# Optimization experiments

Hardware: AMD Instinct MI355X
Metric: run time of the kernel (lower is better)

The kernel has to match this reference:

```python
import jax, jax.numpy as jnp
import numpy as np

B, T, V, E, H, NL = 32, 64, 32000, 300, 512, 2
NF, D = 128, 32  # num midi frames, midi_frame_dim
LSTM_IN = E + D  # 332


def setup_inputs() -> dict:
    key = jax.random.key(0)
    ks = jax.random.split(key, 20)
    s = 0.05
    inp = {
        "input_seq": jax.random.randint(ks[0], (B, T), 0, V),
        "midi_sequence": jax.random.normal(ks[1], (B, NF, D), jnp.float32),
        "emb": jax.random.normal(ks[2], (V, E), jnp.float32) * s,
        "mp_w": jax.random.normal(ks[3], (D, D), jnp.float32) * s,
        "mp_b": jnp.zeros((D,), jnp.float32),
        "wh": jax.random.normal(ks[4], (H, H), jnp.float32) * s,
        "wm": jax.random.normal(ks[5], (H, D), jnp.float32) * s,
        "v": jax.random.normal(ks[6], (1, H), jnp.float32) * s,
        "w_ih0": jax.random.normal(ks[7], (4 * H, LSTM_IN), jnp.float32) * s,
        "w_hh0": jax.random.normal(ks[8], (4 * H, H), jnp.float32) * s,
        "b_ih0": jnp.zeros((4 * H,), jnp.float32),
        "b_hh0": jnp.zeros((4 * H,), jnp.float32),
        "w_ih1": jax.random.normal(ks[9], (4 * H, H), jnp.float32) * s,
        "w_hh1": jax.random.normal(ks[10], (4 * H, H), jnp.float32) * s,
        "b_ih1": jnp.zeros((4 * H,), jnp.float32),
        "b_hh1": jnp.zeros((4 * H,), jnp.float32),
        "fc_w": jax.random.uniform(ks[11], (V, H), jnp.float32, -0.1, 0.1),
        "fc_b": jnp.zeros((V,), jnp.float32),
    }
    return inp


def _lstm_cell(x, hp, cp, wih, whh, bih, bhh):
    # PyTorch gate order: i, f, g, o
    g = x @ wih.T + hp @ whh.T + bih + bhh
    i, f, gg, o = jnp.split(g, 4, axis=-1)
    cn = jax.nn.sigmoid(f) * cp + jax.nn.sigmoid(i) * jnp.tanh(gg)
    hn = jax.nn.sigmoid(o) * jnp.tanh(cn)
    return hn, cn


def reference(input_seq, midi_sequence, emb, mp_w, mp_b, wh, wm, v,
              w_ih0, w_hh0, b_ih0, b_hh0, w_ih1, w_hh1, b_ih1, b_hh1,
              fc_w, fc_b):
    embeddings = emb[input_seq]  # [B,T,E] (dropout = identity in eval)
    midi_proj = jax.nn.relu(jnp.einsum('bfd,ed->bfe', midi_sequence, mp_w) + mp_b)  # [B,NF,D]
    midi_key = jnp.einsum('bfd,hd->bfh', midi_proj, wm)  # precomputed W_m(midi_proj)

    h0 = jnp.zeros((NL, B, H), embeddings.dtype)
    c0 = jnp.zeros((NL, B, H), embeddings.dtype)

    def step(carry, x_t):
        h, c = carry
        h_top = h[-1]  # [B,H]
        energy = jnp.tanh((h_top @ wh.T)[:, None, :] + midi_key)  # [B,NF,H]
        scores = jnp.einsum('bfh,h->bf', energy, v[0])
        attn = jax.nn.softmax(scores, axis=-1)  # [B,NF]
        ctx = jnp.einsum('bf,bfd->bd', attn, midi_proj)  # [B,D]
        x = jnp.concatenate([x_t, ctx], axis=-1)  # [B,E+D]
        h1, c1 = _lstm_cell(x, h[0], c[0], w_ih0, w_hh0, b_ih0, b_hh0)
        h2, c2 = _lstm_cell(h1, h[1], c[1], w_ih1, w_hh1, b_ih1, b_hh1)
        return (jnp.stack([h1, h2]), jnp.stack([c1, c2])), (h2, attn)

    (hF, cF), (outs, attns) = jax.lax.scan(step, (h0, c0), embeddings.transpose(1, 0, 2))
    lstm_out = outs.transpose(1, 0, 2)  # [B,T,H]
    logits = lstm_out @ fc_w.T + fc_b  # [B,T,V]
    return logits, (hF, cF), attns.transpose(1, 0, 2)
```

## Files before the change

### kernel.cpp

```cpp
#include <hip/hip_runtime.h>
#include <hip/hip_bf16.h>

#define Bsz 32
#define Tn  64
#define Vn  32000
#define En  300
#define Hn  512
#define NFn 128
#define Dn  32
#define G4  2048
#define LIN 332
#define NWG 256

#define OFF_MPROJ 0
#define OFF_E0    (OFF_MPROJ + 131072)
#define OFF_PG0B  (OFF_E0 + 4194304)
#define OFF_H1T   (OFF_PG0B + 65536)
#define OFF_H2T0  (OFF_H1T + 16384)
#define OFF_H2T1  (OFF_H2T0 + 16384)
#define OFF_H2BB  (OFF_H2T1 + 16384)
#define OFF_C1T   (OFF_H2BB + 16384)
#define OFF_C2T   (OFF_C1T + 16384)
#define OFF_FLG   (OFF_C2T + 16384)
#define OFF_DONE  (OFF_FLG + 4096)
#define OFF_VC    (OFF_DONE + 256)
#define OFF_MKEY  (OFF_VC + 16)
#define OFF_WHT   (OFF_MKEY + 2097152)
#define OFF_WCTX  (OFF_WHT + 262144)
#define OFF_X     (OFF_WCTX + 65536)
#define OFF_W0    (OFF_X + 655360)
#define OFF_HBF   OFF_X
#define OFF_FCWBF (OFF_X + 524288)

#define O_H1S 0
#define O_H2S 1048576

#define OFF_QS    OFF_PG0B
#define OFF_CTXP  (OFF_PG0B + 16384)
#define OFF_DENP  (OFF_PG0B + 24576)
#define OFF_ES    (OFF_PG0B + 24832)

#define OUT_HF  65536000
#define OUT_CF  65568768
#define OUT_ATT 65601536

#define L_HS2   0
#define L_HS1   4096
#define L_GL    8192
#define L_PG0   8480
#define L_C1    8736
#define L_C2    8800
#define L_CTX   8864
#define L_DEN   9128
#define L_QL    9136
#define L_VL    9664
#define L_SP    10192
#define L_ESL   10464
#define L_CP    10480
#define SCAN_LDS_FLOATS 11024
#define SCAN_LDS_BYTES  (SCAN_LDS_FLOATS*4)

typedef __attribute__((ext_vector_type(8))) short short8;
typedef __attribute__((ext_vector_type(4))) float f32x4;
typedef unsigned short u16;

__device__ __forceinline__ float frcp(float x){ return __builtin_amdgcn_rcpf(x); }
__device__ __forceinline__ float ftanh(float x){
  float e = __expf(2.0f*x);
  return 1.0f - 2.0f*frcp(e+1.0f);
}
__device__ __forceinline__ float fsig(float x){
  return frcp(1.0f + __expf(-x));
}
__device__ __forceinline__ u16 f2bf(float f){
  __hip_bfloat16 h = __float2bfloat16(f);
  u16 r; __builtin_memcpy(&r, &h, 2); return r;
}

__device__ __forceinline__ float ldc1(const float* p){
  return __hip_atomic_load(p, __ATOMIC_RELAXED, __HIP_MEMORY_SCOPE_AGENT);
}
__device__ __forceinline__ void stc1(float* p, float v){
  __hip_atomic_store(p, v, __ATOMIC_RELAXED, __HIP_MEMORY_SCOPE_AGENT);
}

__device__ __forceinline__ void flag_store(float* ws, int c, int slot, float v){
  stc1(ws + OFF_FLG + c*256 + slot*4, v);
}
__device__ __forceinline__ void aggregate(float* ws, int c, float tgt, int tid){
  if (tid < 64){
    const float* fl = ws + OFF_FLG + c*256;
    unsigned cc = 0;
    while (true){
      float v = ldc1(fl + tid*4);
      if (__ballot(v >= tgt) == ~0ull) break;
      __builtin_amdgcn_s_sleep(2);
      if (++cc >= (1u<<20)) break;
    }
    if (tid == 0) stc1(ws + OFF_DONE + c*16, tgt);
  }
}
__device__ __forceinline__ void waitD(float* ws, int c, float tgt){
  __syncthreads();
  if (threadIdx.x == 0){
    unsigned cc = 0;
    while (ldc1(ws + OFF_DONE + c*16) < tgt){
      __builtin_amdgcn_s_sleep(2);
      if (++cc >= (1u<<22)) break;
    }
  }
  __syncthreads();
  asm volatile("" ::: "memory");
}

__device__ __forceinline__ float redux32(float (&v)[32], int L){
  #pragma unroll
  for (int i=0;i<5;i++){
    const int m = 1<<i, h = 16>>i;
    const bool up = (L & m);
    #pragma unroll
    for (int u=0; u<h; u++){
      float send = up ? v[u] : v[u+h];
      float keep = up ? v[u+h] : v[u];
      v[u] = keep + __shfl_xor(send, m, 64);
    }
  }
  v[0] += __shfl_xor(v[0], 32, 64);
  return v[0];
}
__device__ __forceinline__ float redux16(float (&v)[16], int L){
  #pragma unroll
  for (int i=0;i<4;i++){
    const int m = 1<<i, h = 8>>i;
    const bool up = (L & m);
    #pragma unroll
    for (int u=0; u<h; u++){
      float send = up ? v[u] : v[u+h];
      float keep = up ? v[u+h] : v[u];
      v[u] = keep + __shfl_xor(send, m, 64);
    }
  }
  v[0] += __shfl_xor(v[0], 16, 64);
  v[0] += __shfl_xor(v[0], 32, 64);
  return v[0];
}

__global__ __launch_bounds__(1024) void p1_midi(
    const float* __restrict__ midi, const float* __restrict__ mp_w,
    const float* __restrict__ mp_b, const float* __restrict__ wm,
    float* __restrict__ ws)
{
  __shared__ float ms[NFn*Dn];
  __shared__ float pj[NFn*33];
  __shared__ float mpw[Dn*33];
  __shared__ float mpb[Dn];
  int b = blockIdx.x, tid = threadIdx.x;
  for (int i=tid;i<NFn*Dn;i+=1024) ms[i] = midi[b*NFn*Dn + i];
  { int e = tid>>5, d = tid&31; mpw[e*33+d] = mp_w[tid]; }
  if (tid < Dn) mpb[tid] = mp_b[tid];
  __syncthreads();
  float* mproj = ws + OFF_MPROJ;
  for (int i=tid;i<NFn*Dn;i+=1024){
    int f = i>>5, e = i&31;
    float a = mpb[e];
    #pragma unroll
    for (int d=0;d<Dn;d++) a += ms[f*32+d]*mpw[e*33+d];
    a = fmaxf(a, 0.0f);
    pj[f*33+e] = a;
    mproj[b*NFn*Dn + i] = a;
  }
  __syncthreads();
  int h = tid & 511, fh = tid >> 9;
  float wreg[32];
  #pragma unroll
  for (int d=0;d<32;d++) wreg[d] = wm[h*32+d];
  float* mkf = ws + OFF_MKEY + b*(NFn*Hn);
  for (int ff=0; ff<64; ff++){
    int f = fh*64 + ff;
    float a = 0.f;
    #pragma unroll
    for (int d=0;d<32;d++) a += pj[f*33+d]*wreg[d];
    mkf[f*512 + h] = a;
  }
}

__global__ __launch_bounds__(256) void p2a_x(
    const int* __restrict__ seq, const float* __restrict__ emb,
    float* __restrict__ ws)
{
  int idx = blockIdx.x*256 + threadIdx.x;
  int bt = idx / 80, c4 = idx - bt*80;
  int b = bt & 31, t = bt >> 5;
  float4 x = {0.f,0.f,0.f,0.f};
  if (c4 < 75){
    int s = seq[b*Tn + t];
    x = *(const float4*)(emb + (long)s*En + c4*4);
  }
  *(float4*)(ws + OFF_X + bt*320 + c4*4) = x;
}

__global__ __launch_bounds__(256) void p2b_w(
    const float* __restrict__ wih0, float* __restrict__ ws)
{
  int idx = blockIdx.x*256 + threadIdx.x;
  int j = idx / 80, c4 = idx - j*80;
  float4 x = {0.f,0.f,0.f,0.f};
  if (c4 < 75) x = *(const float4*)(wih0 + (long)j*LIN + c4*4);
  *(float4*)(ws + OFF_W0 + j*320 + c4*4) = x;
}

__global__ __launch_bounds__(256) void p2c_e0(
    const float* __restrict__ ws_c, const float* __restrict__ bih0,
    const float* __restrict__ bhh0, float* __restrict__ ws)
{
  const float* A  = ws_c + OFF_W0;
  const float* Bm = ws_c + OFF_X;
  __shared__ float Al[32][132];
  __shared__ float Bl[32][132];
  int tid = threadIdx.x;
  int j0t = blockIdx.x*128, bt0 = blockIdx.y*128;
  int tx = tid & 15, ty = tid >> 4;
  float acc[8][8];
  #pragma unroll
  for (int i=0;i<8;i++)
    #pragma unroll
    for (int j=0;j<8;j++) acc[i][j] = 0.f;

  int m = tid >> 1;
  int kq = (tid & 1) * 16;
  for (int kk=0; kk<320; kk+=32){
    __syncthreads();
    {
      const float* As = A  + (long)(j0t+m)*320 + kk + kq;
      const float* Bs = Bm + (long)(bt0+m)*320 + kk + kq;
      float4 a0 = *(const float4*)(As+0), a1 = *(const float4*)(As+4);
      float4 a2 = *(const float4*)(As+8), a3 = *(const float4*)(As+12);
      float4 b0 = *(const float4*)(Bs+0), b1 = *(const float4*)(Bs+4);
      float4 b2 = *(const float4*)(Bs+8), b3 = *(const float4*)(Bs+12);
      Al[kq+0][m]=a0.x; Al[kq+1][m]=a0.y; Al[kq+2][m]=a0.z; Al[kq+3][m]=a0.w;
      Al[kq+4][m]=a1.x; Al[kq+5][m]=a1.y; Al[kq+6][m]=a1.z; Al[kq+7][m]=a1.w;
      Al[kq+8][m]=a2.x; Al[kq+9][m]=a2.y; Al[kq+10][m]=a2.z; Al[kq+11][m]=a2.w;
      Al[kq+12][m]=a3.x; Al[kq+13][m]=a3.y; Al[kq+14][m]=a3.z; Al[kq+15][m]=a3.w;
      Bl[kq+0][m]=b0.x; Bl[kq+1][m]=b0.y; Bl[kq+2][m]=b0.z; Bl[kq+3][m]=b0.w;
      Bl[kq+4][m]=b1.x; Bl[kq+5][m]=b1.y; Bl[kq+6][m]=b1.z; Bl[kq+7][m]=b1.w;
      Bl[kq+8][m]=b2.x; Bl[kq+9][m]=b2.y; Bl[kq+10][m]=b2.z; Bl[kq+11][m]=b2.w;
      Bl[kq+12][m]=b3.x; Bl[kq+13][m]=b3.y; Bl[kq+14][m]=b3.z; Bl[kq+15][m]=b3.w;
    }
    __syncthreads();
    #pragma unroll 4
    for (int k=0;k<32;k++){
      float4 a0 = *(const float4*)&Al[k][ty*8];
      float4 a1 = *(const float4*)&Al[k][ty*8+4];
      float4 b0 = *(const float4*)&Bl[k][tx*8];
      float4 b1 = *(const float4*)&Bl[k][tx*8+4];
      float av[8] = {a0.x,a0.y,a0.z,a0.w,a1.x,a1.y,a1.z,a1.w};
      float bv[8] = {b0.x,b0.y,b0.z,b0.w,b1.x,b1.y,b1.z,b1.w};
      #pragma unroll
      for (int i=0;i<8;i++)
        #pragma unroll
        for (int j=0;j<8;j++) acc[i][j] += av[i]*bv[j];
    }
  }
  float* E0 = ws + OFF_E0;
  #pragma unroll
  for (int i=0;i<8;i++){
    int j = j0t + ty*8 + i;
    float be = bih0[j] + bhh0[j];
    #pragma unroll
    for (int jj=0;jj<8;jj++){
      int c = bt0 + tx*8 + jj;
      int tt = c >> 5, bb = c & 31;
      E0[tt*65536 + (bb>>3)*16384 + j*8 + (bb&7)] = acc[i][jj] + be;
    }
  }
}

__global__ __launch_bounds__(256) void p3_cvt(
    const float* __restrict__ fcw, float* __restrict__ ws)
{
  u16* dst = (u16*)(ws + OFF_FCWBF);
  int base = (blockIdx.x*256 + threadIdx.x)*8;
  float4 x = *(const float4*)(fcw+base);
  float4 y = *(const float4*)(fcw+base+4);
  short8 p;
  p[0]=(short)f2bf(x.x); p[1]=(short)f2bf(x.y); p[2]=(short)f2bf(x.z); p[3]=(short)f2bf(x.w);
  p[4]=(short)f2bf(y.x); p[5]=(short)f2bf(y.y); p[6]=(short)f2bf(y.z); p[7]=(short)f2bf(y.w);
  *(short8*)(dst+base) = p;
}

__global__ __launch_bounds__(256) void p5_wctx(
    const float* __restrict__ wih0, float* __restrict__ ws)
{
  int idx = blockIdx.x*256 + threadIdx.x;
  int j = idx >> 5, d = idx & 31;
  ws[OFF_WCTX + idx] = wih0[(long)j*LIN + En + d];
}

__global__ __launch_bounds__(512) void p6_vc(
    const float* __restrict__ v, float* __restrict__ ws)
{
  __shared__ float s[8];
  int tid = threadIdx.x;
  float a = fabsf(v[tid]);
  #pragma unroll
  for (int m=1;m<64;m<<=1) a += __shfl_xor(a, m, 64);
  if ((tid&63)==0) s[tid>>6] = a;
  __syncthreads();
  if (tid==0){
    float c=0;
    #pragma unroll
    for (int i=0;i<8;i++) c += s[i];
    ws[OFF_VC] = c;
  }
}

__global__ __launch_bounds__(256) void p0_init(float* __restrict__ ws,
                                               float* __restrict__ out){
  int idx = blockIdx.x*256 + threadIdx.x;
  out[O_H2S + idx] = 0.f;
  if (idx < 4352) ws[OFF_FLG + idx] = 0.f;
}

__global__ __launch_bounds__(256, 1)
void scan_all(
    const float* __restrict__ wih1, const float* __restrict__ whh1,
    const float* __restrict__ whh0, const float* __restrict__ bih1,
    const float* __restrict__ bhh1, const float* __restrict__ wh,
    const float* __restrict__ vvec, float* __restrict__ ws,
    float* __restrict__ out)
{
  extern __shared__ float lds[];
  float* hs2  = lds + L_HS2;
  float* hs1  = lds + L_HS1;
  float* gl   = lds + L_GL;
  float* pg0l = lds + L_PG0;
  float* c1l  = lds + L_C1;
  float* c2l  = lds + L_C2;
  float* ctxl = lds + L_CTX;
  float* denl = lds + L_DEN;
  float* ql   = lds + L_QL;
  float* vl   = lds + L_VL;
  float* sp   = lds + L_SP;
  float* esl  = lds + L_ESL;
  float* cp   = lds + L_CP;

  const int wg = blockIdx.x, tid = threadIdx.x;
  const int rg = wg >> 2, bg = wg & 3;
  const int b2 = wg >> 3, fs = wg & 7;
  const int bgp = wg >> 6;
  const int wv = tid >> 6, L = tid & 63;
  u16* hbf = (u16*)(ws + OFF_HBF);

  float w_a[8][8], w_b[8][8];
  #pragma unroll
  for (int r=0;r<8;r++){
    int row = wv*512 + rg*8 + r;
    #pragma unroll
    for (int j=0;j<8;j++){
      w_a[r][j] = wih1[(long)row*512 + j*64 + L];
      w_b[r][j] = whh1[(long)row*512 + j*64 + L];
    }
  }

  const int s4 = ((L&1)<<3) | ((L&2)<<1) | ((L&4)>>1) | ((L&8)>>3);
  const int q_sr = s4 >> 3, q_sx = s4 & 7;
  const int s5 = ((L&1)<<4) | ((L&2)<<2) | (L&4) | ((L&8)>>2) | ((L&16)>>4);
  const int r_sr = s5 >> 3, r_sx = s5 & 7;
  float bsum[2]; int glIdx[2], pgIdx[2];
  #pragma unroll
  for (int p=0;p<2;p++){
    int kk = p*4 + r_sr;
    int row = wv*512 + rg*8 + kk;
    bsum[p] = bih1[row] + bhh1[row];
    glIdx[p] = (wv*8 + kk)*9 + r_sx;
    pgIdx[p] = (wv*8 + kk)*8 + r_sx;
  }

  if (tid < 64){ c1l[tid] = 0.f; c2l[tid] = 0.f; }
  {
    int r = tid>>3, bb = tid&7;
    int row = ((r>>3)<<9) + rg*8 + (r&7);
    pg0l[r*8+bb] = ws[OFF_E0 + bg*16384 + row*8 + bb];
  }
  vl[tid + (tid>>5)] = vvec[tid];
  { int t2 = tid + 256; vl[t2 + (t2>>5)] = vvec[t2]; }
  const float Cv = ws[OFF_VC];
  __syncthreads();

  for (int t=0; t<64; t++){
    const float tgt = (float)(t+1);
    if (t > 0) waitD(ws, 0+bg, (float)t);
    {
      const float* h2b = out + O_H2S + t*16384 + bg*4096;
      float4 v0 = *(const float4*)(h2b +    0 + tid*4);
      float4 v1 = *(const float4*)(h2b + 1024 + tid*4);
      float4 v2 = *(const float4*)(h2b + 2048 + tid*4);
      float4 v3 = *(const float4*)(h2b + 3072 + tid*4);
      int kb = tid >> 1, bb0 = (tid&1)*4;
      hs2[(bb0+0)*512 +   0 + kb] = v0.x; hs2[(bb0+1)*512 +   0 + kb] = v0.y;
      hs2[(bb0+2)*512 +   0 + kb] = v0.z; hs2[(bb0+3)*512 +   0 + kb] = v0.w;
      hs2[(bb0+0)*512 + 128 + kb] = v1.x; hs2[(bb0+1)*512 + 128 + kb] = v1.y;
      hs2[(bb0+2)*512 + 128 + kb] = v1.z; hs2[(bb0+3)*512 + 128 + kb] = v1.w;
      hs2[(bb0+0)*512 + 256 + kb] = v2.x; hs2[(bb0+1)*512 + 256 + kb] = v2.y;
      hs2[(bb0+2)*512 + 256 + kb] = v2.z; hs2[(bb0+3)*512 + 256 + kb] = v2.w;
      hs2[(bb0+0)*512 + 384 + kb] = v3.x; hs2[(bb0+1)*512 + 384 + kb] = v3.y;
      hs2[(bb0+2)*512 + 384 + kb] = v3.z; hs2[(bb0+3)*512 + 384 + kb] = v3.w;
    }
    __syncthreads();
    {
      const float* w0p = wh + (long)(rg*8 + wv*2)*512;
      const float* w1p = w0p + 512;
      float vq[16];
      #pragma unroll
      for (int i=0;i<16;i++) vq[i] = 0.f;
      #pragma unroll
      for (int j=0;j<8;j++){
        int k = j*64 + L;
        float wa = w0p[k], wb = w1p[k];
        #pragma unroll
        for (int x=0;x<8;x++){
          float hv = hs2[x*512+k];
          vq[x] += wa*hv; vq[8+x] += wb*hv;
        }
      }
      float qv = redux16(vq, L);
      if (L < 16)
        stc1(ws + OFF_QS + (bg*8+q_sx)*512 + rg*8 + wv*2 + q_sr, qv);
    }
    __syncthreads();
    if (tid == 0) flag_store(ws, 4+bg, wg>>2, tgt);
    if (wg < 4) aggregate(ws, 4+wg, tgt, tid);

    waitD(ws, 4+bgp, tgt);
    ql[tid + (tid>>5)] = ldc1(ws + OFF_QS + b2*512 + tid);
    { int t2 = tid + 256; ql[t2 + (t2>>5)] = ldc1(ws + OFF_QS + b2*512 + t2); }
    __syncthreads();
    {
      int f = tid>>4, hg = tid&15;
      const float* mkr = ws + OFF_MKEY + b2*65536 + (fs*16+f)*512 + hg*32;
      const float* qb = ql + hg*33;
      const float* vb = vl + hg*33;
      float s = 0.f;
      #pragma unroll
      for (int c=0; c<32; c+=4){
        float4 m4 = *(const float4*)(mkr+c);
        s += vb[c+0]*ftanh(qb[c+0]+m4.x) + vb[c+1]*ftanh(qb[c+1]+m4.y)
           + vb[c+2]*ftanh(qb[c+2]+m4.z) + vb[c+3]*ftanh(qb[c+3]+m4.w);
      }
      sp[f*17+hg] = s;
    }
    __syncthreads();
    if (tid < 16){
      float s = 0.f;
      #pragma unroll
      for (int g=0; g<16; g++) s += sp[tid*17+g];
      float e = __expf(s - Cv);
      esl[tid] = e;
      stc1(ws + OFF_ES + b2*128 + fs*16 + tid, e);
    }
    __syncthreads();
    if (tid == 0){
      float d = 0.f;
      #pragma unroll
      for (int i=0;i<16;i++) d += esl[i];
      stc1(ws + OFF_DENP + b2*8 + fs, d);
    }
    {
      int d2 = tid&31, f0 = tid>>5;
      cp[d2*17+f0]   = esl[f0]  * ws[OFF_MPROJ + b2*4096 + (fs*16+f0)*32   + d2];
      cp[d2*17+f0+8] = esl[f0+8]* ws[OFF_MPROJ + b2*4096 + (fs*16+f0+8)*32 + d2];
    }
    __syncthreads();
    if (tid < 32){
      float s = 0.f;
      #pragma unroll
      for (int ff=0; ff<16; ff++) s += cp[tid*17+ff];
      stc1(ws + OFF_CTXP + b2*256 + fs*32 + tid, s);
    }
    __syncthreads();
    if (tid == 0) flag_store(ws, 8+bgp, wg&63, tgt);
    if ((wg&63) == 0) aggregate(ws, 8+bgp, tgt, tid);

    waitD(ws, 8+bg, tgt);
    if (tid < 8){
      float dsum = 0.f;
      #pragma unroll
      for (int f2=0; f2<8; f2++) dsum += ldc1(ws + OFF_DENP + (bg*8+tid)*8 + f2);
      denl[tid] = frcp(dsum);
    }
    __syncthreads();
    {
      int bb = tid>>5, d = tid&31;
      float s = 0.f;
      #pragma unroll
      for (int f2=0; f2<8; f2++) s += ldc1(ws + OFF_CTXP + (bg*8+bb)*256 + f2*32 + d);
      ctxl[bb*33+d] = s * denl[bb];
    }
    if (rg == 0){
      #pragma unroll
      for (int i0=0; i0<4; i0++){
        int i = tid + i0*256;
        int bb = i>>7, f = i&127;
        float e = ldc1(ws + OFF_ES + (bg*8+bb)*128 + f);
        __builtin_nontemporal_store(e * denl[bb],
            out + OUT_ATT + (bg*8+bb)*8192 + t*128 + f);
      }
    }
    __syncthreads();
    {
      int r = tid>>3, bb = tid&7;
      int row = ((r>>3)<<9) + rg*8 + (r&7);
      float g0 = pg0l[r*8+bb];
      const float* wr = ws + OFF_WCTX + row*32;
      #pragma unroll
      for (int d2=0; d2<32; d2+=4){
        float4 w4 = *(const float4*)(wr+d2);
        g0 += w4.x*ctxl[bb*33+d2] + w4.y*ctxl[bb*33+d2+1]
            + w4.z*ctxl[bb*33+d2+2] + w4.w*ctxl[bb*33+d2+3];
      }
      gl[r*9+bb] = g0;
    }
    __syncthreads();
    if (tid < 64){
      int kk = tid>>3, bb = tid&7;
      float gi = gl[(kk)*9+bb],     gf = gl[(8+kk)*9+bb];
      float gg2 = gl[(16+kk)*9+bb], go = gl[(24+kk)*9+bb];
      float cp2 = c1l[tid];
      float cn = fsig(gf)*cp2 + fsig(gi)*ftanh(gg2);
      float hn = fsig(go)*ftanh(cn);
      c1l[tid] = cn;
      stc1(out + O_H1S + t*16384 + bg*4096 + (rg*8+kk)*8 + bb, hn);
      if (t == 63){
        int bgl = bg*8+bb, kgl = rg*8+kk;
        __builtin_nontemporal_store(hn, out + OUT_HF + bgl*512 + kgl);
        __builtin_nontemporal_store(cn, out + OUT_CF + bgl*512 + kgl);
      }
    }
    __syncthreads();
    if (tid == 0) flag_store(ws, 12+bg, wg>>2, tgt);
    if (wg < 4) aggregate(ws, 12+wg, tgt, tid);

    waitD(ws, 12+bg, tgt);
    {
      const float* h1b = out + O_H1S + t*16384 + bg*4096;
      float4 v0 = *(const float4*)(h1b +    0 + tid*4);
      float4 v1 = *(const float4*)(h1b + 1024 + tid*4);
      float4 v2 = *(const float4*)(h1b + 2048 + tid*4);
      float4 v3 = *(const float4*)(h1b + 3072 + tid*4);
      int kb = tid >> 1, bb0 = (tid&1)*4;
      hs1[(bb0+0)*512 +   0 + kb] = v0.x; hs1[(bb0+1)*512 +   0 + kb] = v0.y;
      hs1[(bb0+2)*512 +   0 + kb] = v0.z; hs1[(bb0+3)*512 +   0 + kb] = v0.w;
      hs1[(bb0+0)*512 + 128 + kb] = v1.x; hs1[(bb0+1)*512 + 128 + kb] = v1.y;
      hs1[(bb0+2)*512 + 128 + kb] = v1.z; hs1[(bb0+3)*512 + 128 + kb] = v1.w;
      hs1[(bb0+0)*512 + 256 + kb] = v2.x; hs1[(bb0+1)*512 + 256 + kb] = v2.y;
      hs1[(bb0+2)*512 + 256 + kb] = v2.z; hs1[(bb0+3)*512 + 256 + kb] = v2.w;
      hs1[(bb0+0)*512 + 384 + kb] = v3.x; hs1[(bb0+1)*512 + 384 + kb] = v3.y;
      hs1[(bb0+2)*512 + 384 + kb] = v3.z; hs1[(bb0+3)*512 + 384 + kb] = v3.w;
    }
    __syncthreads();
    #pragma unroll
    for (int p=0; p<2; p++){
      float vals[32];
      #pragma unroll
      for (int i=0;i<32;i++) vals[i] = 0.f;
      #pragma unroll
      for (int j=0;j<8;j++){
        int k = j*64 + L;
        float h1v[8], h2v[8];
        #pragma unroll
        for (int x=0;x<8;x++){ h1v[x] = hs1[x*512+k]; h2v[x] = hs2[x*512+k]; }
        #pragma unroll
        for (int r=0;r<4;r++){
          const float wa = w_a[p*4+r][j], wb = w_b[p*4+r][j];
          #pragma unroll
          for (int x=0;x<8;x++) vals[r*8+x] += wa*h1v[x] + wb*h2v[x];
        }
      }
      float v0 = redux32(vals, L);
      if (L < 32) gl[glIdx[p]] = v0 + bsum[p];
    }
    __syncthreads();
    if (tid < 64){
      int kk = tid>>3, bb = tid&7;
      float gi = gl[(kk)*9+bb],     gf = gl[(8+kk)*9+bb];
      float gg2 = gl[(16+kk)*9+bb], go = gl[(24+kk)*9+bb];
      float cp3 = c2l[tid];
      float cn = fsig(gf)*cp3 + fsig(gi)*ftanh(gg2);
      float hn = fsig(go)*ftanh(cn);
      c2l[tid] = cn;
      int k2 = rg*8+kk, b = bg*8+bb;
      stc1(out + O_H2S + (t+1)*16384 + bg*4096 + k2*8 + bb, hn);
      __builtin_nontemporal_store(f2bf(hn), hbf + (t*32+b)*512 + k2);
      if (t == 63){
        __builtin_nontemporal_store(hn, out + OUT_HF + 16384 + b*512 + k2);
        __builtin_nontemporal_store(cn, out + OUT_CF + 16384 + b*512 + k2);
      }
    }
    __syncthreads();
    if (tid == 0) flag_store(ws, 0+bg, wg>>2, tgt);
    if (wg < 4) aggregate(ws, 0+wg, tgt, tid);

    if (t < 63){
      #pragma unroll
      for (int p=0; p<2; p++){
        float vals[32];
        #pragma unroll
        for (int i=0;i<32;i++) vals[i] = 0.f;
        #pragma unroll
        for (int j=0;j<8;j++){
          int k = j*64 + L;
          float h1v[8];
          #pragma unroll
          for (int x=0;x<8;x++) h1v[x] = hs1[x*512+k];
          #pragma unroll
          for (int r=0;r<4;r++){
            int row = wv*512 + rg*8 + p*4 + r;
            const float wc = whh0[(long)row*512 + k];
            #pragma unroll
            for (int x=0;x<8;x++) vals[r*8+x] += wc*h1v[x];
          }
        }
        float v0 = redux32(vals, L);
        if (L < 32) pg0l[pgIdx[p]] = v0;
      }
      __syncthreads();
      {
        int r = tid>>3, bb = tid&7;
        int row = ((r>>3)<<9) + rg*8 + (r&7);
        pg0l[r*8+bb] += ws[OFF_E0 + (t+1)*65536 + bg*16384 + row*8 + bb];
      }
    }
  }
}

__global__ __launch_bounds__(256) void fc_gemm(
    const float* __restrict__ ws_f, const float* __restrict__ fcb,
    float* __restrict__ out)
{
  const u16* A  = (const u16*)(ws_f + OFF_FCWBF);
  const u16* Bm = (const u16*)(ws_f + OFF_HBF);
  __shared__ u16 Al[128*40];
  __shared__ u16 Bl[128*40];
  int tid = threadIdx.x;
  int v0 = blockIdx.x*128, bt0 = blockIdx.y*128;
  int lane = tid & 63, wv = tid >> 6;
  int wr = wv >> 1, wc = wv & 1;
  f32x4 acc[4][4];
  #pragma unroll
  for (int i=0;i<4;i++)
    #pragma unroll
    for (int j=0;j<4;j++) acc[i][j] = (f32x4){0.f,0.f,0.f,0.f};

  int ar = wr*64 + (lane&15);
  int br = wc*64 + (lane&15);
  int ks = (lane>>4)*8;

  for (int kk=0; kk<512; kk+=32){
    __syncthreads();
    #pragma unroll
    for (int i=0;i<2;i++){
      int ld = tid + 256*i;
      int row = ld >> 2, cs = (ld & 3)*8;
      *(int4*)(&Al[row*40+cs]) = *(const int4*)(A  + (v0+row)*512 + kk + cs);
      *(int4*)(&Bl[row*40+cs]) = *(const int4*)(Bm + (bt0+row)*512 + kk + cs);
    }
    __syncthreads();
    short8 af[4], bf[4];
    #pragma unroll
    for (int m=0;m<4;m++) af[m] = *(const short8*)(&Al[(ar+m*16)*40 + ks]);
    #pragma unroll
    for (int n=0;n<4;n++) bf[n] = *(const short8*)(&Bl[(br+n*16)*40 + ks]);
    #pragma unroll
    for (int m=0;m<4;m++)
      #pragma unroll
      for (int n=0;n<4;n++)
        acc[m][n] = __builtin_amdgcn_mfma_f32_16x16x32_bf16(af[m], bf[n], acc[m][n], 0,0,0);
  }
  int r4 = (lane>>4)*4;
  #pragma unroll
  for (int m=0;m<4;m++){
    int v = v0 + wr*64 + m*16 + r4;
    float4 bias = *(const float4*)(fcb + v);
    #pragma unroll
    for (int n=0;n<4;n++){
      int bt = bt0 + wc*64 + n*16 + (lane&15);
      int b = bt & 31, t = bt >> 5;
      f32x4 a = acc[m][n];
      float4 res = { a[0]+bias.x, a[1]+bias.y, a[2]+bias.z, a[3]+bias.w };
      *(float4*)(out + b*2048000 + t*32000 + v) = res;
    }
  }
}

extern "C" void kernel_launch(void* const* d_in, const int* in_sizes, int n_in,
                              void* d_out, int out_size, void* d_ws, size_t ws_size,
                              hipStream_t stream)
{
  const int*   seq  = (const int*)d_in[0];
  const float* midi = (const float*)d_in[1];
  const float* emb  = (const float*)d_in[2];
  const float* mpw  = (const float*)d_in[3];
  const float* mpb  = (const float*)d_in[4];
  const float* wh   = (const float*)d_in[5];
  const float* wm   = (const float*)d_in[6];
  const float* vv   = (const float*)d_in[7];
  const float* wih0 = (const float*)d_in[8];
  const float* whh0 = (const float*)d_in[9];
  const float* bih0 = (const float*)d_in[10];
  const float* bhh0 = (const float*)d_in[11];
  const float* wih1 = (const float*)d_in[12];
  const float* whh1 = (const float*)d_in[13];
  const float* bih1 = (const float*)d_in[14];
  const float* bhh1 = (const float*)d_in[15];
  const float* fcw  = (const float*)d_in[16];
  const float* fcb  = (const float*)d_in[17];
  float* out = (float*)d_out;
  float* ws  = (float*)d_ws;

  p1_midi<<<32, 1024, 0, stream>>>(midi, mpw, mpb, wm, ws);
  p2a_x  <<<640, 256, 0, stream>>>(seq, emb, ws);
  p2b_w  <<<640, 256, 0, stream>>>(wih0, ws);
  p2c_e0 <<<dim3(16,16), 256, 0, stream>>>(ws, bih0, bhh0, ws);
  p3_cvt <<<8000, 256, 0, stream>>>(fcw, ws);
  p5_wctx<<<256, 256, 0, stream>>>(wih0, ws);
  p6_vc  <<<1, 512, 0, stream>>>(vv, ws);
  p0_init<<<64, 256, 0, stream>>>(ws, out);

  scan_all<<<NWG, 256, SCAN_LDS_BYTES, stream>>>(wih1, whh1, whh0, bih1, bhh1,
                                                 wh, vv, ws, out);

  fc_gemm<<<dim3(250,16), 256, 0, stream>>>(ws, fcb, out);
}
```

Baseline: 5.908 ms.

## Cache W_hh0 slice in LDS and use per-timestep exchange buffers

Each workgroup now loads its 32-row slice of W_hh0 into shared memory once before the scan, so the per-step layer-0 recurrent product reads weights from LDS rather than from global memory. Dynamic LDS grows to about 107 KB and the max dynamic shared memory attribute is raised to allow it. The cross-workgroup exchange buffers for attention queries, exp-scores, denominators and context partials move to per-timestep slots inside the unused logits region of the output buffer. With no slot reused across steps, write-after-read hazards go away, and the readers switch from cache-bypassing loads to plain loads. The risk is that plain loads could return stale cached data, and the logits region must be fully overwritten later by the FC GEMM.

```diff
diff --git a/kernel.cpp b/kernel.cpp
--- a/kernel.cpp
+++ b/kernel.cpp
@@ -32,13 +32,12 @@
 #define OFF_HBF   OFF_X
 #define OFF_FCWBF (OFF_X + 524288)
 
-#define O_H1S 0
-#define O_H2S 1048576
-
-#define OFF_QS    OFF_PG0B
-#define OFF_CTXP  (OFF_PG0B + 16384)
-#define OFF_DENP  (OFF_PG0B + 24576)
-#define OFF_ES    (OFF_PG0B + 24832)
+#define O_H1S  0
+#define O_H2S  1048576
+#define O_QS   2113536
+#define O_CTXP 3162112
+#define O_DENP 3686400
+#define O_ES   3702784
 
 #define OUT_HF  65536000
 #define OUT_CF  65568768
@@ -57,7 +56,8 @@
 #define L_SP    10192
 #define L_ESL   10464
 #define L_CP    10480
-#define SCAN_LDS_FLOATS 11024
+#define L_W0    11024
+#define SCAN_LDS_FLOATS 27408
 #define SCAN_LDS_BYTES  (SCAN_LDS_FLOATS*4)
 
 typedef __attribute__((ext_vector_type(8))) short short8;
@@ -343,6 +343,7 @@
   float* sp   = lds + L_SP;
   float* esl  = lds + L_ESL;
   float* cp   = lds + L_CP;
+  float* w0l  = lds + L_W0;
 
   const int wg = blockIdx.x, tid = threadIdx.x;
   const int rg = wg >> 2, bg = wg & 3;
@@ -360,6 +361,12 @@
       w_a[r][j] = wih1[(long)row*512 + j*64 + L];
       w_b[r][j] = whh1[(long)row*512 + j*64 + L];
     }
+  }
+  for (int c=0; c<64; c++){
+    int idx = c*256 + tid;
+    int lr = idx >> 9, k = idx & 511;
+    int grow = (lr>>3)*512 + rg*8 + (lr&7);
+    w0l[idx] = whh0[(long)grow*512 + k];
   }
 
   const int s4 = ((L&1)<<3) | ((L&2)<<1) | ((L&4)>>1) | ((L&8)>>3);
@@ -425,15 +432,15 @@
       }
       float qv = redux16(vq, L);
       if (L < 16)
-        stc1(ws + OFF_QS + (bg*8+q_sx)*512 + rg*8 + wv*2 + q_sr, qv);
+        stc1(out + O_QS + t*16384 + (bg*8+q_sx)*512 + rg*8 + wv*2 + q_sr, qv);
     }
     __syncthreads();
     if (tid == 0) flag_store(ws, 4+bg, wg>>2, tgt);
     if (wg < 4) aggregate(ws, 4+wg, tgt, tid);
 
     waitD(ws, 4+bgp, tgt);
-    ql[tid + (tid>>5)] = ldc1(ws + OFF_QS + b2*512 + tid);
-    { int t2 = tid + 256; ql[t2 + (t2>>5)] = ldc1(ws + OFF_QS + b2*512 + t2); }
+    ql[tid + (tid>>5)] = out[O_QS + t*16384 + b2*512 + tid];
+    { int t2 = tid + 256; ql[t2 + (t2>>5)] = out[O_QS + t*16384 + b2*512 + t2]; }
     __syncthreads();
     {
       int f = tid>>4, hg = tid&15;
@@ -456,14 +463,14 @@
       for (int g=0; g<16; g++) s += sp[tid*17+g];
       float e = __expf(s - Cv);
       esl[tid] = e;
-      stc1(ws + OFF_ES + b2*128 + fs*16 + tid, e);
+      stc1(out + O_ES + t*4096 + b2*128 + fs*16 + tid, e);
     }
     __syncthreads();
     if (tid == 0){
       float d = 0.f;
       #pragma unroll
       for (int i=0;i<16;i++) d += esl[i];
-      stc1(ws + OFF_DENP + b2*8 + fs, d);
+      stc1(out + O_DENP + t*256 + b2*8 + fs, d);
     }
     {
       int d2 = tid&31, f0 = tid>>5;
@@ -475,7 +482,7 @@
       float s = 0.f;
       #pragma unroll
       for (int ff=0; ff<16; ff++) s += cp[tid*17+ff];
-      stc1(ws + OFF_CTXP + b2*256 + fs*32 + tid, s);
+      stc1(out + O_CTXP + t*8192 + b2*256 + fs*32 + tid, s);
     }
     __syncthreads();
     if (tid == 0) flag_store(ws, 8+bgp, wg&63, tgt);
@@ -485,7 +492,7 @@
     if (tid < 8){
       float dsum = 0.f;
       #pragma unroll
-      for (int f2=0; f2<8; f2++) dsum += ldc1(ws + OFF_DENP + (bg*8+tid)*8 + f2);
+      for (int f2=0; f2<8; f2++) dsum += out[O_DENP + t*256 + (bg*8+tid)*8 + f2];
       denl[tid] = frcp(dsum);
     }
     __syncthreads();
@@ -493,7 +500,7 @@
       int bb = tid>>5, d = tid&31;
       float s = 0.f;
       #pragma unroll
-      for (int f2=0; f2<8; f2++) s += ldc1(ws + OFF_CTXP + (bg*8+bb)*256 + f2*32 + d);
+      for (int f2=0; f2<8; f2++) s += out[O_CTXP + t*8192 + (bg*8+bb)*256 + f2*32 + d];
       ctxl[bb*33+d] = s * denl[bb];
     }
     if (rg == 0){
@@ -501,7 +508,7 @@
       for (int i0=0; i0<4; i0++){
         int i = tid + i0*256;
         int bb = i>>7, f = i&127;
-        float e = ldc1(ws + OFF_ES + (bg*8+bb)*128 + f);
+        float e = out[O_ES + t*4096 + (bg*8+bb)*128 + f];
         __builtin_nontemporal_store(e * denl[bb],
             out + OUT_ATT + (bg*8+bb)*8192 + t*128 + f);
       }
@@ -614,8 +621,7 @@
           for (int x=0;x<8;x++) h1v[x] = hs1[x*512+k];
           #pragma unroll
           for (int r=0;r<4;r++){
-            int row = wv*512 + rg*8 + p*4 + r;
-            const float wc = whh0[(long)row*512 + k];
+            const float wc = w0l[(wv*8 + p*4 + r)*512 + k];
             #pragma unroll
             for (int x=0;x<8;x++) vals[r*8+x] += wc*h1v[x];
           }
@@ -717,6 +723,10 @@
   float* out = (float*)d_out;
   float* ws  = (float*)d_ws;
 
+  hipFuncSetAttribute((const void*)scan_all,
+                      hipFuncAttributeMaxDynamicSharedMemorySize,
+                      SCAN_LDS_BYTES);
+
   p1_midi<<<32, 1024, 0, stream>>>(midi, mpw, mpb, wm, ws);
   p2a_x  <<<640, 256, 0, stream>>>(seq, emb, ws);
   p2b_w  <<<640, 256, 0, stream>>>(wih0, ws);
```

After: 5.662 ms. -4.2%, faster.
